# Kernel optimization log

Measured on AMD Instinct MI355X. Metric: run time of the kernel, lower is better.

The kernel has to match this reference:

```python
import jax, jax.numpy as jnp
import numpy as np

# ---- sRGB <-> CIELAB (D65) helpers, matching standard torch lab2rgb/rgb2lab ----
_RGB2XYZ = jnp.array([[0.412453, 0.357580, 0.180423],
                      [0.212671, 0.715160, 0.072169],
                      [0.019334, 0.119193, 0.950227]], dtype=jnp.float32)
_XYZ2RGB = jnp.array([[ 3.2404542, -1.5371385, -0.4985314],
                      [-0.9692660,  1.8760108,  0.0415560],
                      [ 0.0556434, -0.2040259,  1.0572252]], dtype=jnp.float32)
_WHITE = jnp.array([0.95047, 1.0, 1.08883], dtype=jnp.float32)
_EPS = 0.008856      # (6/29)^3
_KAPPA = 7.787

def _srgb_to_linear(c):
    safe = jnp.maximum(c, 0.04045)
    return jnp.where(c <= 0.04045, c / 12.92, ((safe + 0.055) / 1.055) ** 2.4)

def _linear_to_srgb(c):
    safe = jnp.maximum(c, 0.0031308)
    return jnp.where(c <= 0.0031308, 12.92 * c, 1.055 * safe ** (1.0 / 2.4) - 0.055)

def rgb2lab(rgb):
    lin = _srgb_to_linear(rgb)                      # [N,3]
    xyz = (lin @ _RGB2XYZ.T) / _WHITE               # [N,3]
    safe = jnp.maximum(xyz, _EPS)
    f = jnp.where(xyz > _EPS, jnp.cbrt(safe), _KAPPA * xyz + 16.0 / 116.0)
    fx, fy, fz = f[..., 0], f[..., 1], f[..., 2]
    L = 116.0 * fy - 16.0
    a = 500.0 * (fx - fy)
    b = 200.0 * (fy - fz)
    return jnp.stack([L, a, b], axis=-1)

def lab2rgb(lab):
    L, a, b = lab[..., 0], lab[..., 1], lab[..., 2]
    fy = (L + 16.0) / 116.0
    fx = fy + a / 500.0
    fz = fy - b / 200.0
    f = jnp.stack([fx, fy, fz], axis=-1)
    f3 = f ** 3
    t = jnp.where(f3 > _EPS, f3, (f - 16.0 / 116.0) / _KAPPA)
    xyz = t * _WHITE
    lin = xyz @ _XYZ2RGB.T
    return _linear_to_srgb(lin)

def _forward(x, w_seq1, b_seq1, w_seq2, b_seq2, w_lin, b_lin,
             w_comb, b_comb, w_logd, b_logd, w_final, b_final):
    # lab branch
    seq = jnp.tanh(x @ w_seq1 + b_seq1) @ w_seq2 + b_seq2        # [N,3]
    lin = x @ w_lin + b_lin                                      # [N,3]
    final_lab = jnp.concatenate([lin, seq], axis=-1) @ w_comb + b_comb
    # log-density branch
    x_rgb = lab2rgb(x)
    log_density = -jnp.log10(x_rgb)
    model_processed = log_density @ w_logd + b_logd
    back_to_lab = rgb2lab(10.0 ** model_processed)
    return jnp.concatenate([final_lab, back_to_lab], axis=-1) @ w_final + b_final


def setup_inputs() -> dict:
    key = jax.random.key(0)
    ks = jax.random.split(key, 13)
    N, H = 2_097_152, 64

    def lin_init(kw, kb, fan_in, fan_out):
        bound = 1.0 / np.sqrt(fan_in)
        w = jax.random.uniform(kw, (fan_in, fan_out), minval=-bound, maxval=bound, dtype=jnp.float32)
        b = jax.random.uniform(kb, (fan_out,), minval=-bound, maxval=bound, dtype=jnp.float32)
        return w, b

    # valid Lab inputs: sample sRGB away from 0/1 then convert
    rgb = jax.random.uniform(ks[0], (N, 3), minval=0.05, maxval=0.95, dtype=jnp.float32)
    x = rgb2lab(rgb)

    kk = jax.random.split(ks[1], 12)
    w_seq1, b_seq1 = lin_init(kk[0], kk[1], 3, H)
    w_seq2, b_seq2 = lin_init(kk[2], kk[3], H, 3)
    w_lin, b_lin = lin_init(kk[4], kk[5], 3, 3)
    w_comb, b_comb = lin_init(kk[6], kk[7], 6, 3)
    w_logd, b_logd = lin_init(kk[8], kk[9], 3, 3)
    w_final, b_final = lin_init(kk[10], kk[11], 6, 3)
    return {"x": x,
            "w_seq1": w_seq1, "b_seq1": b_seq1, "w_seq2": w_seq2, "b_seq2": b_seq2,
            "w_lin": w_lin, "b_lin": b_lin, "w_comb": w_comb, "b_comb": b_comb,
            "w_logd": w_logd, "b_logd": b_logd, "w_final": w_final, "b_final": b_final}


def reference(x, w_seq1, b_seq1, w_seq2, b_seq2, w_lin, b_lin,
              w_comb, b_comb, w_logd, b_logd, w_final, b_final):
    return _forward(x, w_seq1, b_seq1, w_seq2, b_seq2, w_lin, b_lin,
                    w_comb, b_comb, w_logd, b_logd, w_final, b_final)
```

## Files before the change

### kernel.cpp

```cpp
#include <hip/hip_runtime.h>

typedef float    v2f __attribute__((ext_vector_type(2)));
typedef _Float16 v2h __attribute__((ext_vector_type(2)));

__device__ __forceinline__ float fexp2(float x) { return __builtin_amdgcn_exp2f(x); }
__device__ __forceinline__ float flog2(float x) { return __builtin_amdgcn_logf(x); }
__device__ __forceinline__ float ffma (float a, float b, float c) { return __builtin_fmaf(a, b, c); }
__device__ __forceinline__ v2f  splat(float s) { v2f v; v.x = s; v.y = s; return v; }
__device__ __forceinline__ v2f  pkfma(v2f a, v2f b, v2f c) { return __builtin_elementwise_fma(a, b, c); }
__device__ __forceinline__ v2h  splath(float s) { v2h v; v.x = (_Float16)s; v.y = (_Float16)s; return v; }
__device__ __forceinline__ v2h  pkfmah(v2h a, v2h b, v2h c) { return __builtin_elementwise_fma(a, b, c); }
__device__ __forceinline__ v2h  cvt_pk(float a, float b) {
    return __builtin_bit_cast(v2h, __builtin_amdgcn_cvt_pkrtz(a, b));
}

#define LAB_EPS 0.008856f
#define F16_116 0.13793103448275862f

__global__ __launch_bounds__(256) void fused_kernel(
    const float* __restrict__ x,
    const float* __restrict__ w_seq1, const float* __restrict__ b_seq1,
    const float* __restrict__ w_seq2, const float* __restrict__ b_seq2,
    const float* __restrict__ w_lin,  const float* __restrict__ b_lin,
    const float* __restrict__ w_comb, const float* __restrict__ b_comb,
    const float* __restrict__ w_logd, const float* __restrict__ b_logd,
    const float* __restrict__ w_final,const float* __restrict__ b_final,
    float* __restrict__ out, int n)
{
    __shared__ float4 wldsa[64];
    __shared__ uint4  wldsb[64];
    __shared__ float  smlds[33];

    const int tid = threadIdx.x;
    if (tid < 64) {
        const int j = tid;
        float H3[9];
        for (int i = 0; i < 3; ++i)
            for (int c = 0; c < 3; ++c) {
                float h = 0.f;
                for (int m = 0; m < 3; ++m) h += w_comb[(i + 3) * 3 + m] * w_final[m * 3 + c];
                H3[i * 3 + c] = h;
            }
        const float w0 = w_seq2[j * 3 + 0], w1 = w_seq2[j * 3 + 1], w2 = w_seq2[j * 3 + 2];
        wldsa[j] = make_float4(w_seq1[j], w_seq1[64 + j], w_seq1[128 + j], b_seq1[j]);
        const float wp0 = w0 * H3[0] + w1 * H3[3] + w2 * H3[6];
        const float wp1 = w0 * H3[1] + w1 * H3[4] + w2 * H3[7];
        const float wp2 = w0 * H3[2] + w1 * H3[5] + w2 * H3[8];
        uint4 wb;
        wb.x = __builtin_bit_cast(unsigned, cvt_pk(wp0, wp0));
        wb.y = __builtin_bit_cast(unsigned, cvt_pk(wp1, wp1));
        wb.z = __builtin_bit_cast(unsigned, cvt_pk(wp2, wp2));
        wb.w = 0u;
        wldsb[j] = wb;
        if (j == 0) {
            float G[9], Wfb[9];
            for (int i = 0; i < 3; ++i)
                for (int c = 0; c < 3; ++c) {
                    float gg = 0.f;
                    for (int m = 0; m < 3; ++m) gg += w_comb[i * 3 + m] * w_final[m * 3 + c];
                    G[i * 3 + c] = gg;
                }
            for (int k = 0; k < 3; ++k)
                for (int c = 0; c < 3; ++c) {
                    float s = 0.f;
                    for (int i = 0; i < 3; ++i) s += w_lin[k * 3 + i] * G[i * 3 + c];
                    smlds[k * 3 + c] = s;
                    Wfb[k * 3 + c]   = w_final[(k + 3) * 3 + c];
                    smlds[18 + k * 3 + c] = w_logd[k * 3 + c];
                }
            for (int c = 0; c < 3; ++c) {
                smlds[9 + c]     = 500.0f * Wfb[3 + c];
                smlds[9 + 3 + c] = 116.0f * Wfb[c] - 500.0f * Wfb[3 + c] + 200.0f * Wfb[6 + c];
                smlds[9 + 6 + c] = -200.0f * Wfb[6 + c];
                float s = b_final[c] - 16.0f * Wfb[c];
                for (int i = 0; i < 3; ++i)
                    s += b_lin[i] * G[i * 3 + c] + b_seq2[i] * H3[i * 3 + c]
                       + b_comb[i] * w_final[i * 3 + c];
                smlds[27 + c] = b_logd[c];
                smlds[30 + c] = s;
            }
        }
    }
    __syncthreads();

    const int g = blockIdx.x * blockDim.x + tid;
    if (g * 2 >= n) return;

    const float2* xin = reinterpret_cast<const float2*>(x) + (size_t)g * 3;
    const float2 v0 = xin[0], v1 = xin[1], v2 = xin[2];
    v2f xs2[3];
    xs2[0].x = v0.x; xs2[0].y = v1.y;
    xs2[1].x = v0.y; xs2[1].y = v2.x;
    xs2[2].x = v1.x; xs2[2].y = v2.y;

    v2h acch[3];
#pragma unroll
    for (int c = 0; c < 3; ++c) acch[c] = splath(0.f);

#pragma unroll 4
    for (int j = 0; j < 64; ++j) {
        const float4 wa = wldsa[j];
        const uint4  wb = wldsb[j];
        v2f t = pkfma(xs2[0], splat(wa.x),
                pkfma(xs2[1], splat(wa.y),
                pkfma(xs2[2], splat(wa.z), splat(wa.w))));
        v2h th = cvt_pk(t.x, t.y);
        th = __builtin_elementwise_min(__builtin_elementwise_max(th, splath(-3.0f)), splath(3.0f));
        const v2h u = th * th;
        v2h P = pkfmah(splath(-0.00120984f), u, splath(0.02603622f));
        P = pkfmah(P, u, splath(-0.20598500f));
        P = pkfmah(P, u, splath(0.95858467f));
        const v2h h = th * P;
        acch[0] = pkfmah(h, __builtin_bit_cast(v2h, wb.x), acch[0]);
        acch[1] = pkfmah(h, __builtin_bit_cast(v2h, wb.y), acch[1]);
        acch[2] = pkfmah(h, __builtin_bit_cast(v2h, wb.z), acch[2]);
    }

    float A[9], U[9], Wld[9], bld[3], cv[3];
#pragma unroll
    for (int i = 0; i < 9; ++i) { A[i] = smlds[i]; U[i] = smlds[9 + i]; Wld[i] = smlds[18 + i]; }
#pragma unroll
    for (int i = 0; i < 3; ++i) { bld[i] = smlds[27 + i]; cv[i] = smlds[30 + i]; }

    float ov[6];
#pragma unroll
    for (int p = 0; p < 2; ++p) {
        const float L  = p ? xs2[0].y : xs2[0].x;
        const float aa = p ? xs2[1].y : xs2[1].x;
        const float bb = p ? xs2[2].y : xs2[2].x;
        const float a0 = p ? (float)acch[0].y : (float)acch[0].x;
        const float a1 = p ? (float)acch[1].y : (float)acch[1].x;
        const float a2 = p ? (float)acch[2].y : (float)acch[2].x;
        const float fy = (L + 16.0f) * (1.0f / 116.0f);
        const float fx = ffma(aa,  0.002f, fy);
        const float fz = ffma(bb, -0.005f, fy);
        float rgb[3];
        {
            const float f3x = fx * fx * fx, f3y = fy * fy * fy, f3z = fz * fz * fz;
            const float tx = f3x > LAB_EPS ? f3x : (fx - F16_116) * (1.0f / 7.787f);
            const float ty = f3y > LAB_EPS ? f3y : (fy - F16_116) * (1.0f / 7.787f);
            const float tz = f3z > LAB_EPS ? f3z : (fz - F16_116) * (1.0f / 7.787f);
            const float X = tx * 0.95047f, Y = ty, Z = tz * 1.08883f;
            const float linv[3] = {
                 3.2404542f * X - 1.5371385f * Y - 0.4985314f * Z,
                -0.9692660f * X + 1.8760108f * Y + 0.0415560f * Z,
                 0.0556434f * X - 0.2040259f * Y + 1.0572252f * Z};
#pragma unroll
            for (int c = 0; c < 3; ++c) {
                const float cc = linv[c];
                const float lo = 12.92f * cc;
                const float hi = ffma(1.055f,
                                      fexp2(flog2(fmaxf(cc, 0.0031308f)) * (1.0f / 2.4f)),
                                      -0.055f);
                rgb[c] = cc <= 0.0031308f ? lo : hi;
            }
        }
        const float ld0 = -0.30102999566398120f * flog2(rgb[0]);
        const float ld1 = -0.30102999566398120f * flog2(rgb[1]);
        const float ld2 = -0.30102999566398120f * flog2(rgb[2]);
        float lin2[3];
#pragma unroll
        for (int c = 0; c < 3; ++c) {
            const float mp  = ffma(ld0, Wld[c], ffma(ld1, Wld[3 + c], ffma(ld2, Wld[6 + c], bld[c])));
            const float r10 = fexp2(mp * 3.3219280948873623f);
            const float lo  = r10 * (1.0f / 12.92f);
            const float base = (fmaxf(r10, 0.04045f) + 0.055f) * (1.0f / 1.055f);
            const float hi  = fexp2(2.4f * flog2(base));
            lin2[c] = r10 <= 0.04045f ? lo : hi;
        }
        const float X2 = (0.412453f * lin2[0] + 0.357580f * lin2[1] + 0.180423f * lin2[2]) * (1.0f / 0.95047f);
        const float Y2 =  0.212671f * lin2[0] + 0.715160f * lin2[1] + 0.072169f * lin2[2];
        const float Z2 = (0.019334f * lin2[0] + 0.119193f * lin2[1] + 0.950227f * lin2[2]) * (1.0f / 1.08883f);
        const float fX = X2 > LAB_EPS ? fexp2(flog2(fmaxf(X2, LAB_EPS)) * (1.0f / 3.0f)) : ffma(7.787f, X2, F16_116);
        const float fY = Y2 > LAB_EPS ? fexp2(flog2(fmaxf(Y2, LAB_EPS)) * (1.0f / 3.0f)) : ffma(7.787f, Y2, F16_116);
        const float fZ = Z2 > LAB_EPS ? fexp2(flog2(fmaxf(Z2, LAB_EPS)) * (1.0f / 3.0f)) : ffma(7.787f, Z2, F16_116);
#pragma unroll
        for (int c = 0; c < 3; ++c) {
            float o = cv[c];
            o = ffma(L,  A[c],     o);
            o = ffma(aa, A[3 + c], o);
            o = ffma(bb, A[6 + c], o);
            o += (c == 0 ? a0 : (c == 1 ? a1 : a2));
            o = ffma(fX, U[c],     o);
            o = ffma(fY, U[3 + c], o);
            o = ffma(fZ, U[6 + c], o);
            ov[p * 3 + c] = o;
        }
    }

    float2* op = reinterpret_cast<float2*>(out) + (size_t)g * 3;
    op[0] = make_float2(ov[0], ov[1]);
    op[1] = make_float2(ov[2], ov[3]);
    op[2] = make_float2(ov[4], ov[5]);
}

extern "C" void kernel_launch(void* const* d_in, const int* in_sizes, int n_in,
                              void* d_out, int out_size, void* d_ws, size_t ws_size,
                              hipStream_t stream)
{
    const float* x       = (const float*)d_in[0];
    const float* w_seq1  = (const float*)d_in[1];
    const float* b_seq1  = (const float*)d_in[2];
    const float* w_seq2  = (const float*)d_in[3];
    const float* b_seq2  = (const float*)d_in[4];
    const float* w_lin   = (const float*)d_in[5];
    const float* b_lin   = (const float*)d_in[6];
    const float* w_comb  = (const float*)d_in[7];
    const float* b_comb  = (const float*)d_in[8];
    const float* w_logd  = (const float*)d_in[9];
    const float* b_logd  = (const float*)d_in[10];
    const float* w_final = (const float*)d_in[11];
    const float* b_final = (const float*)d_in[12];
    float* outp = (float*)d_out;

    const int n = in_sizes[0] / 3;
    const int threads = 256;
    const int total_threads = (n + 1) / 2;
    const int blocks = (total_threads + threads - 1) / threads;

    fused_kernel<<<blocks, threads, 0, stream>>>(
        x, w_seq1, b_seq1, w_seq2, b_seq2, w_lin, b_lin, w_comb, b_comb,
        w_logd, b_logd, w_final, b_final, outp, n);
}
```

Before: 135.4 us.

## Move per-block weight folding into a separate prep kernel reading from global memory

Weight folding was recomputed by every block into shared memory, followed by a block barrier. It now runs once in a one-block prep kernel that writes a global workspace, and the main kernel reads weights from that workspace (likely scalar/constant-cache loads) without LDS or __syncthreads. The log10 and 10^x constants are also folded into the pre-negated, pre-scaled logd weights and bias, removing a few multiplies per pixel. The cost is an extra kernel launch and per-iteration global (cached) loads instead of LDS reads in the 64-step loop.

```diff
diff --git a/kernel.cpp b/kernel.cpp
--- a/kernel.cpp
+++ b/kernel.cpp
@@ -16,74 +16,89 @@
 
 #define LAB_EPS 0.008856f
 #define F16_116 0.13793103448275862f
-
-__global__ __launch_bounds__(256) void fused_kernel(
-    const float* __restrict__ x,
+#define LOG2_10 3.3219280948873623f
+
+__device__ __align__(16) float g_ws[548];
+
+__global__ __launch_bounds__(64) void prep_kernel(
     const float* __restrict__ w_seq1, const float* __restrict__ b_seq1,
     const float* __restrict__ w_seq2, const float* __restrict__ b_seq2,
     const float* __restrict__ w_lin,  const float* __restrict__ b_lin,
     const float* __restrict__ w_comb, const float* __restrict__ b_comb,
     const float* __restrict__ w_logd, const float* __restrict__ b_logd,
-    const float* __restrict__ w_final,const float* __restrict__ b_final,
+    const float* __restrict__ w_final,const float* __restrict__ b_final)
+{
+    const int j = threadIdx.x;
+    float H3[9];
+#pragma unroll
+    for (int i = 0; i < 3; ++i)
+#pragma unroll
+        for (int c = 0; c < 3; ++c) {
+            float h = 0.f;
+            for (int m = 0; m < 3; ++m) h += w_comb[(i + 3) * 3 + m] * w_final[m * 3 + c];
+            H3[i * 3 + c] = h;
+        }
+
+    float4* wsa = reinterpret_cast<float4*>(g_ws);
+    uint4*  wsb = reinterpret_cast<uint4*>(g_ws) + 64;
+
+    wsa[j] = make_float4(w_seq1[j], w_seq1[64 + j], w_seq1[128 + j], b_seq1[j]);
+    const float w0 = w_seq2[j * 3 + 0], w1 = w_seq2[j * 3 + 1], w2 = w_seq2[j * 3 + 2];
+    const float wp0 = w0 * H3[0] + w1 * H3[3] + w2 * H3[6];
+    const float wp1 = w0 * H3[1] + w1 * H3[4] + w2 * H3[7];
+    const float wp2 = w0 * H3[2] + w1 * H3[5] + w2 * H3[8];
+    uint4 wb;
+    wb.x = __builtin_bit_cast(unsigned, cvt_pk(wp0, wp0));
+    wb.y = __builtin_bit_cast(unsigned, cvt_pk(wp1, wp1));
+    wb.z = __builtin_bit_cast(unsigned, cvt_pk(wp2, wp2));
+    wb.w = 0u;
+    wsb[j] = wb;
+
+    if (j == 0) {
+        float* sm = g_ws + 512;
+        float G[9], Wfb[9];
+#pragma unroll
+        for (int i = 0; i < 3; ++i)
+#pragma unroll
+            for (int c = 0; c < 3; ++c) {
+                float gg = 0.f;
+                for (int m = 0; m < 3; ++m) gg += w_comb[i * 3 + m] * w_final[m * 3 + c];
+                G[i * 3 + c] = gg;
+            }
+#pragma unroll
+        for (int k = 0; k < 3; ++k)
+#pragma unroll
+            for (int c = 0; c < 3; ++c) {
+                float s = 0.f;
+                for (int i = 0; i < 3; ++i) s += w_lin[k * 3 + i] * G[i * 3 + c];
+                sm[k * 3 + c]      = s;
+                Wfb[k * 3 + c]     = w_final[(k + 3) * 3 + c];
+                sm[18 + k * 3 + c] = -w_logd[k * 3 + c];
+            }
+#pragma unroll
+        for (int c = 0; c < 3; ++c) {
+            sm[9 + c]     = 500.0f * Wfb[3 + c];
+            sm[9 + 3 + c] = 116.0f * Wfb[c] - 500.0f * Wfb[3 + c] + 200.0f * Wfb[6 + c];
+            sm[9 + 6 + c] = -200.0f * Wfb[6 + c];
+            float s = b_final[c] - 16.0f * Wfb[c];
+            for (int i = 0; i < 3; ++i)
+                s += b_lin[i] * G[i * 3 + c] + b_seq2[i] * H3[i * 3 + c]
+                   + b_comb[i] * w_final[i * 3 + c];
+            sm[27 + c] = LOG2_10 * b_logd[c];
+            sm[30 + c] = s;
+        }
+    }
+}
+
+__global__ __launch_bounds__(256) void fused_kernel(
+    const float* __restrict__ x,
     float* __restrict__ out, int n)
 {
-    __shared__ float4 wldsa[64];
-    __shared__ uint4  wldsb[64];
-    __shared__ float  smlds[33];
-
-    const int tid = threadIdx.x;
-    if (tid < 64) {
-        const int j = tid;
-        float H3[9];
-        for (int i = 0; i < 3; ++i)
-            for (int c = 0; c < 3; ++c) {
-                float h = 0.f;
-                for (int m = 0; m < 3; ++m) h += w_comb[(i + 3) * 3 + m] * w_final[m * 3 + c];
-                H3[i * 3 + c] = h;
-            }
-        const float w0 = w_seq2[j * 3 + 0], w1 = w_seq2[j * 3 + 1], w2 = w_seq2[j * 3 + 2];
-        wldsa[j] = make_float4(w_seq1[j], w_seq1[64 + j], w_seq1[128 + j], b_seq1[j]);
-        const float wp0 = w0 * H3[0] + w1 * H3[3] + w2 * H3[6];
-        const float wp1 = w0 * H3[1] + w1 * H3[4] + w2 * H3[7];
-        const float wp2 = w0 * H3[2] + w1 * H3[5] + w2 * H3[8];
-        uint4 wb;
-        wb.x = __builtin_bit_cast(unsigned, cvt_pk(wp0, wp0));
-        wb.y = __builtin_bit_cast(unsigned, cvt_pk(wp1, wp1));
-        wb.z = __builtin_bit_cast(unsigned, cvt_pk(wp2, wp2));
-        wb.w = 0u;
-        wldsb[j] = wb;
-        if (j == 0) {
-            float G[9], Wfb[9];
-            for (int i = 0; i < 3; ++i)
-                for (int c = 0; c < 3; ++c) {
-                    float gg = 0.f;
-                    for (int m = 0; m < 3; ++m) gg += w_comb[i * 3 + m] * w_final[m * 3 + c];
-                    G[i * 3 + c] = gg;
-                }
-            for (int k = 0; k < 3; ++k)
-                for (int c = 0; c < 3; ++c) {
-                    float s = 0.f;
-                    for (int i = 0; i < 3; ++i) s += w_lin[k * 3 + i] * G[i * 3 + c];
-                    smlds[k * 3 + c] = s;
-                    Wfb[k * 3 + c]   = w_final[(k + 3) * 3 + c];
-                    smlds[18 + k * 3 + c] = w_logd[k * 3 + c];
-                }
-            for (int c = 0; c < 3; ++c) {
-                smlds[9 + c]     = 500.0f * Wfb[3 + c];
-                smlds[9 + 3 + c] = 116.0f * Wfb[c] - 500.0f * Wfb[3 + c] + 200.0f * Wfb[6 + c];
-                smlds[9 + 6 + c] = -200.0f * Wfb[6 + c];
-                float s = b_final[c] - 16.0f * Wfb[c];
-                for (int i = 0; i < 3; ++i)
-                    s += b_lin[i] * G[i * 3 + c] + b_seq2[i] * H3[i * 3 + c]
-                       + b_comb[i] * w_final[i * 3 + c];
-                smlds[27 + c] = b_logd[c];
-                smlds[30 + c] = s;
-            }
-        }
-    }
-    __syncthreads();
-
-    const int g = blockIdx.x * blockDim.x + tid;
+    const float4* __restrict__ wsa = reinterpret_cast<const float4*>(g_ws);
+    const uint4*  __restrict__ wsb = reinterpret_cast<const uint4*>(g_ws) + 64;
+    const float*  __restrict__ wse = g_ws + 512;
+
+    const int g = blockIdx.x * blockDim.x + threadIdx.x;
     if (g * 2 >= n) return;
 
     const float2* xin = reinterpret_cast<const float2*>(x) + (size_t)g * 3;
@@ -99,8 +114,8 @@
 
 #pragma unroll 4
     for (int j = 0; j < 64; ++j) {
-        const float4 wa = wldsa[j];
-        const uint4  wb = wldsb[j];
+        const float4 wa = wsa[j];
+        const uint4  wb = wsb[j];
         v2f t = pkfma(xs2[0], splat(wa.x),
                 pkfma(xs2[1], splat(wa.y),
                 pkfma(xs2[2], splat(wa.z), splat(wa.w))));
@@ -116,11 +131,11 @@
         acch[2] = pkfmah(h, __builtin_bit_cast(v2h, wb.z), acch[2]);
     }
 
-    float A[9], U[9], Wld[9], bld[3], cv[3];
-#pragma unroll
-    for (int i = 0; i < 9; ++i) { A[i] = smlds[i]; U[i] = smlds[9 + i]; Wld[i] = smlds[18 + i]; }
-#pragma unroll
-    for (int i = 0; i < 3; ++i) { bld[i] = smlds[27 + i]; cv[i] = smlds[30 + i]; }
+    float A[9], U[9], Wn[9], bl2[3], cv[3];
+#pragma unroll
+    for (int i = 0; i < 9; ++i) { A[i] = wse[i]; U[i] = wse[9 + i]; Wn[i] = wse[18 + i]; }
+#pragma unroll
+    for (int i = 0; i < 3; ++i) { bl2[i] = wse[27 + i]; cv[i] = wse[30 + i]; }
 
     float ov[6];
 #pragma unroll
@@ -155,14 +170,14 @@
                 rgb[c] = cc <= 0.0031308f ? lo : hi;
             }
         }
-        const float ld0 = -0.30102999566398120f * flog2(rgb[0]);
-        const float ld1 = -0.30102999566398120f * flog2(rgb[1]);
-        const float ld2 = -0.30102999566398120f * flog2(rgb[2]);
+        const float lg0 = flog2(rgb[0]);
+        const float lg1 = flog2(rgb[1]);
+        const float lg2 = flog2(rgb[2]);
         float lin2[3];
 #pragma unroll
         for (int c = 0; c < 3; ++c) {
-            const float mp  = ffma(ld0, Wld[c], ffma(ld1, Wld[3 + c], ffma(ld2, Wld[6 + c], bld[c])));
-            const float r10 = fexp2(mp * 3.3219280948873623f);
+            const float e   = ffma(lg0, Wn[c], ffma(lg1, Wn[3 + c], ffma(lg2, Wn[6 + c], bl2[c])));
+            const float r10 = fexp2(e);
             const float lo  = r10 * (1.0f / 12.92f);
             const float base = (fmaxf(r10, 0.04045f) + 0.055f) * (1.0f / 1.055f);
             const float hi  = fexp2(2.4f * flog2(base));
@@ -218,7 +233,8 @@
     const int total_threads = (n + 1) / 2;
     const int blocks = (total_threads + threads - 1) / threads;
 
-    fused_kernel<<<blocks, threads, 0, stream>>>(
-        x, w_seq1, b_seq1, w_seq2, b_seq2, w_lin, b_lin, w_comb, b_comb,
-        w_logd, b_logd, w_final, b_final, outp, n);
-}
+    prep_kernel<<<1, 64, 0, stream>>>(
+        w_seq1, b_seq1, w_seq2, b_seq2, w_lin, b_lin, w_comb, b_comb,
+        w_logd, b_logd, w_final, b_final);
+    fused_kernel<<<blocks, threads, 0, stream>>>(x, outp, n);
+}
```

New measurement: 137.2 us. About the same (+1.3%).
